# Performance work log

Measured on AMD Instinct MI355X. Metric: run time of the kernel, lower is better.

The kernel has to match this reference:

```python
import jax, jax.numpy as jnp
import numpy as np

EMBED_DIM = 4096
LOW_RANK = 512
BATCH = 8192
K_SEL = 128


def setup_inputs() -> dict:
    key = jax.random.key(0)
    k1, k2, k3, k4 = jax.random.split(key, 4)
    base = jax.random.normal(k1, (BATCH, EMBED_DIM), dtype=jnp.float32)
    source = jax.random.normal(k2, (BATCH, EMBED_DIM), dtype=jnp.float32)
    # fast path: only subspaces[0] is used (all examples share the same index set)
    row = jax.random.randint(k3, (1, K_SEL), 0, LOW_RANK)
    subspaces = jnp.broadcast_to(row, (BATCH, K_SEL)).astype(jnp.int64)
    # orthogonal (column-orthonormal) rotation weight, as produced by
    # torch.nn.utils.parametrizations.orthogonal on [embed_dim, low_rank]
    W, _ = jnp.linalg.qr(jax.random.normal(k4, (EMBED_DIM, LOW_RANK), dtype=jnp.float32))
    return {"base": base, "source": source, "subspaces": subspaces, "W": W}


def reference(base, source, subspaces, W):
    # rotated_base / rotated_source: [B, r]
    # diff in rotated space, gather selected subspace columns, project back.
    sel = subspaces[0]                      # [k] shared index set (fast path)
    diff = (source - base) @ W              # [B, r]
    diff_sel = diff[:, sel]                 # [B, k]
    W_sel = W[:, sel]                       # [d, k]
    out = base + diff_sel @ W_sel.T         # [B, d]
    return out.astype(base.dtype)
```

## Files before the change

### kernel.cpp

```cpp
#include <hip/hip_runtime.h>
#include <hip/hip_bf16.h>

typedef __attribute__((ext_vector_type(4))) float  f32x4;
typedef __attribute__((ext_vector_type(8))) short  short8;
typedef __attribute__((ext_vector_type(4))) short  short4v;

#define EMBED 4096
#define LR    512
#define KSEL  128
#define BATCH 8192
#define NSLICE 8
#define KSLICE 512

__device__ __forceinline__ short f2bf(float x) {
  union { float f; unsigned u; } c; c.f = x;
  unsigned r = c.u + 0x7FFFu + ((c.u >> 16) & 1u);
  return (short)(r >> 16);
}
__device__ __forceinline__ float bf2f(short s) {
  union { unsigned u; float f; } c; c.u = ((unsigned)(unsigned short)s) << 16;
  return c.f;
}
__device__ __forceinline__ void storept(float* p, float v) { *p = v; }
__device__ __forceinline__ void storept(short* p, float v) { *p = f2bf(v); }
__device__ __forceinline__ void loadpart(const float* p, f32x4& a, f32x4& b) {
  a += *(const f32x4*)p; b += *(const f32x4*)(p + 4);
}
__device__ __forceinline__ void loadpart(const short* p, f32x4& a, f32x4& b) {
  short8 v = *(const short8*)p;
  #pragma unroll
  for (int j = 0; j < 4; ++j) { a[j] += bf2f(v[j]); b[j] += bf2f(v[4 + j]); }
}

__global__ __launch_bounds__(256) void pack_w_kernel(
    const float* __restrict__ W, const int* __restrict__ sel,
    short* __restrict__ Wp, short* __restrict__ Wtp) {
  int idx = blockIdx.x * 256 + threadIdx.x;
  int e = idx >> 7;
  int c = idx & 127;
  int r = sel[c];
  short v = f2bf(W[e * LR + r]);
  Wp [(((e >> 3) << 7) + c) * 8 + (e & 7)] = v;
  Wtp[(((c >> 3) << 12) + e) * 8 + (c & 7)] = v;
}

template<typename PT>
__global__ __launch_bounds__(512, 4) void gemm1a_kernel(
    const float* __restrict__ base, const float* __restrict__ src,
    const short* __restrict__ Wp, PT* __restrict__ Tpart) {
  __shared__ __align__(16) short D[2 * 2048];
  const int t  = threadIdx.x;
  const int w  = t >> 6, l = t & 63;
  const int lr = l & 15, lg = l >> 4;
  const int rg = blockIdx.x & 63, slice = blockIdx.x >> 6;
  const int row0 = rg * 128;
  const int k0 = slice * KSLICE;

  short8 bfr[16];
  #pragma unroll
  for (int kg = 0; kg < 16; ++kg)
    bfr[kg] = *(const short8*)(Wp + (((((k0 >> 3) + kg * 4 + lg)) << 7) + w * 16 + lr) * 8);

  const int srow  = t >> 5;
  const int sbyte = srow * 256 + ((((t & 31) >> 1) ^ (srow & 7)) << 4) + (t & 1) * 8;
  const float* bp = base + (size_t)(row0 + srow) * EMBED + k0 + (t & 31) * 4;
  const float* sp = src  + (size_t)(row0 + srow) * EMBED + k0 + (t & 31) * 4;

  const int rsw = (lr & 7) << 4;
  const char* tb = (const char*)D + lr * 256;

  f32x4 vbA = *(const f32x4*)bp,          vsA = *(const f32x4*)sp;
  f32x4 vbB = *(const f32x4*)(bp + 128),  vsB = *(const f32x4*)(sp + 128);

  f32x4 acc = {0.f, 0.f, 0.f, 0.f};
  PT* tout = Tpart + (size_t)slice * BATCH * KSEL + (size_t)(row0 + lg * 4) * KSEL + w * 16 + lr;

  #define KSTEP(BUF, VB, VS, KG0, PF_OK, PF_OFF)                              \
    do {                                                                      \
      short4v d;                                                              \
      _Pragma("unroll")                                                       \
      for (int j = 0; j < 4; ++j) d[j] = f2bf(VS[j] - VB[j]);                 \
      *(short4v*)((char*)D + (BUF) * 4096 + sbyte) = d;                       \
      if (PF_OK) {                                                            \
        VB = *(const f32x4*)(bt + (PF_OFF));                                  \
        VS = *(const f32x4*)(st + (PF_OFF));                                  \
      }                                                                       \
      __syncthreads();                                                        \
      _Pragma("unroll")                                                       \
      for (int kg = 0; kg < 4; ++kg) {                                        \
        short8 a = *(const short8*)(tb + (BUF) * 4096 +                       \
                                    ((kg * 64 + lg * 16) ^ rsw));             \
        acc = __builtin_amdgcn_mfma_f32_16x16x32_bf16(a, bfr[(KG0) + kg],     \
                                                      acc, 0, 0, 0);          \
      }                                                                       \
    } while (0)

  for (int tile = 0; tile < 8; ++tile) {
    const float* bt = bp + (size_t)tile * 16 * EMBED;
    const float* st = sp + (size_t)tile * 16 * EMBED;
    const bool pf = (tile < 7);
    KSTEP(0, vbA, vsA, 0,  true, 256);
    KSTEP(1, vbB, vsB, 4,  true, 384);
    KSTEP(0, vbA, vsA, 8,  pf,   16 * EMBED);
    KSTEP(1, vbB, vsB, 12, pf,   16 * EMBED + 128);
    PT* o = tout + (size_t)tile * 16 * KSEL;
    #pragma unroll
    for (int r = 0; r < 4; ++r) storept(o + (size_t)r * KSEL, acc[r]);
    acc = (f32x4){0.f, 0.f, 0.f, 0.f};
  }
  #undef KSTEP
}

template<typename PT>
__global__ __launch_bounds__(512) void reduce_kernel(
    const PT* __restrict__ Tpart, short* __restrict__ Tp) {
  const int tid = blockIdx.x * 512 + threadIdx.x;
  const int kkg = tid & 15, row = tid >> 4;
  f32x4 s0 = {0.f, 0.f, 0.f, 0.f}, s1 = {0.f, 0.f, 0.f, 0.f};
  #pragma unroll
  for (int s = 0; s < NSLICE; ++s)
    loadpart(Tpart + ((size_t)s * BATCH + row) * KSEL + kkg * 8, s0, s1);
  short8 o;
  #pragma unroll
  for (int j = 0; j < 4; ++j) { o[j] = f2bf(s0[j]); o[4 + j] = f2bf(s1[j]); }
  *(short8*)(Tp + ((size_t)kkg * BATCH + row) * 8) = o;
}

__global__ __launch_bounds__(256) void gemm2_kernel(
    const float* __restrict__ base, const short* __restrict__ Tp,
    const short* __restrict__ Wtp, float* __restrict__ out) {
  const int t  = threadIdx.x;
  const int w  = t >> 6, l = t & 63;
  const int lr = l & 15, lg = l >> 4;
  const int mt = blockIdx.x >> 4, nt = blockIdx.x & 15;
  const int row0 = mt * 64;
  const int col0 = nt * 256 + w * 64;

  short8 afr[4][4];
  #pragma unroll
  for (int m = 0; m < 4; ++m)
    #pragma unroll
    for (int ks = 0; ks < 4; ++ks)
      afr[m][ks] = *(const short8*)(Tp + (size_t)(((ks * 4 + lg) << 13) + row0 + m * 16 + lr) * 8);

  f32x4 acc[4][4];
  #pragma unroll
  for (int m = 0; m < 4; ++m)
    #pragma unroll
    for (int nf = 0; nf < 4; ++nf) acc[m][nf] = (f32x4){0.f, 0.f, 0.f, 0.f};

  #pragma unroll
  for (int nf = 0; nf < 4; ++nf) {
    short8 bfr[4];
    #pragma unroll
    for (int ks = 0; ks < 4; ++ks)
      bfr[ks] = *(const short8*)(Wtp + (size_t)(((ks * 4 + lg) << 12) + col0 + nf * 16 + lr) * 8);
    #pragma unroll
    for (int m = 0; m < 4; ++m)
      #pragma unroll
      for (int ks = 0; ks < 4; ++ks)
        acc[m][nf] = __builtin_amdgcn_mfma_f32_16x16x32_bf16(afr[m][ks], bfr[ks], acc[m][nf], 0, 0, 0);
  }

  #pragma unroll
  for (int m = 0; m < 4; ++m)
    #pragma unroll
    for (int r = 0; r < 4; ++r) {
      const size_t row = row0 + m * 16 + lg * 4 + r;
      #pragma unroll
      for (int nf = 0; nf < 4; ++nf) {
        const size_t o = row * EMBED + col0 + nf * 16 + lr;
        out[o] = base[o] + acc[m][nf][r];
      }
    }
}

extern "C" void kernel_launch(void* const* d_in, const int* in_sizes, int n_in,
                              void* d_out, int out_size, void* d_ws, size_t ws_size,
                              hipStream_t stream) {
  const float* base = (const float*)d_in[0];
  const float* src  = (const float*)d_in[1];
  const int*   sub  = (const int*)d_in[2];
  const float* W    = (const float*)d_in[3];
  float* out = (float*)d_out;

  short* Wp  = (short*)d_ws;
  short* Wtp = Wp  + EMBED * KSEL;
  short* Tp  = Wtp + EMBED * KSEL;
  char*  rest = (char*)(Tp + BATCH * KSEL);

  pack_w_kernel<<<EMBED * KSEL / 256, 256, 0, stream>>>(W, sub, Wp, Wtp);

  const size_t need_f32 = (size_t)4 * 1024 * 1024 +
                          (size_t)NSLICE * BATCH * KSEL * sizeof(float);
  if (ws_size >= need_f32) {
    float* Tpart = (float*)rest;
    gemm1a_kernel<float><<<512, 512, 0, stream>>>(base, src, Wp, Tpart);
    reduce_kernel<float><<<BATCH * 16 / 512, 512, 0, stream>>>(Tpart, Tp);
  } else {
    short* Tpart = (short*)rest;
    gemm1a_kernel<short><<<512, 512, 0, stream>>>(base, src, Wp, Tpart);
    reduce_kernel<short><<<BATCH * 16 / 512, 512, 0, stream>>>(Tpart, Tp);
  }

  gemm2_kernel<<<(BATCH / 64) * 16, 256, 0, stream>>>(base, Tp, Wtp, out);
}
```

Measured before the change: 126.0 us.

## Load activation diff directly into MFMA A-fragments, dropping LDS staging in gemm1

```diff
diff --git a/kernel.cpp b/kernel.cpp
--- a/kernel.cpp
+++ b/kernel.cpp
@@ -3,7 +3,6 @@
 
 typedef __attribute__((ext_vector_type(4))) float  f32x4;
 typedef __attribute__((ext_vector_type(8))) short  short8;
-typedef __attribute__((ext_vector_type(4))) short  short4v;
 
 #define EMBED 4096
 #define LR    512
@@ -48,67 +47,45 @@
 __global__ __launch_bounds__(512, 4) void gemm1a_kernel(
     const float* __restrict__ base, const float* __restrict__ src,
     const short* __restrict__ Wp, PT* __restrict__ Tpart) {
-  __shared__ __align__(16) short D[2 * 2048];
   const int t  = threadIdx.x;
   const int w  = t >> 6, l = t & 63;
   const int lr = l & 15, lg = l >> 4;
   const int rg = blockIdx.x & 63, slice = blockIdx.x >> 6;
-  const int row0 = rg * 128;
+  const int row0 = rg * 128 + w * 16;
   const int k0 = slice * KSLICE;
 
-  short8 bfr[16];
+  const float* bp = base + (size_t)(row0 + lr) * EMBED + k0 + lg * 8;
+  const float* sp = src  + (size_t)(row0 + lr) * EMBED + k0 + lg * 8;
+  const short8* wq = (const short8*)Wp + ((k0 >> 3) + lg) * 128 + lr;
+
+  f32x4 acc[8];
   #pragma unroll
-  for (int kg = 0; kg < 16; ++kg)
-    bfr[kg] = *(const short8*)(Wp + (((((k0 >> 3) + kg * 4 + lg)) << 7) + w * 16 + lr) * 8);
+  for (int c = 0; c < 8; ++c) acc[c] = (f32x4){0.f, 0.f, 0.f, 0.f};
 
-  const int srow  = t >> 5;
-  const int sbyte = srow * 256 + ((((t & 31) >> 1) ^ (srow & 7)) << 4) + (t & 1) * 8;
-  const float* bp = base + (size_t)(row0 + srow) * EMBED + k0 + (t & 31) * 4;
-  const float* sp = src  + (size_t)(row0 + srow) * EMBED + k0 + (t & 31) * 4;
+  #pragma unroll
+  for (int ks = 0; ks < 16; ++ks) {
+    f32x4 b0 = *(const f32x4*)(bp + ks * 32);
+    f32x4 b1 = *(const f32x4*)(bp + ks * 32 + 4);
+    f32x4 s0 = *(const f32x4*)(sp + ks * 32);
+    f32x4 s1 = *(const f32x4*)(sp + ks * 32 + 4);
+    union { short8 v; __hip_bfloat162 h[4]; } ua;
+    ua.h[0] = __float22bfloat162_rn(make_float2(s0[0] - b0[0], s0[1] - b0[1]));
+    ua.h[1] = __float22bfloat162_rn(make_float2(s0[2] - b0[2], s0[3] - b0[3]));
+    ua.h[2] = __float22bfloat162_rn(make_float2(s1[0] - b1[0], s1[1] - b1[1]));
+    ua.h[3] = __float22bfloat162_rn(make_float2(s1[2] - b1[2], s1[3] - b1[3]));
+    #pragma unroll
+    for (int c = 0; c < 8; ++c) {
+      short8 bf = wq[ks * 512 + c * 16];
+      acc[c] = __builtin_amdgcn_mfma_f32_16x16x32_bf16(ua.v, bf, acc[c], 0, 0, 0);
+    }
+  }
 
-  const int rsw = (lr & 7) << 4;
-  const char* tb = (const char*)D + lr * 256;
-
-  f32x4 vbA = *(const f32x4*)bp,          vsA = *(const f32x4*)sp;
-  f32x4 vbB = *(const f32x4*)(bp + 128),  vsB = *(const f32x4*)(sp + 128);
-
-  f32x4 acc = {0.f, 0.f, 0.f, 0.f};
-  PT* tout = Tpart + (size_t)slice * BATCH * KSEL + (size_t)(row0 + lg * 4) * KSEL + w * 16 + lr;
-
-  #define KSTEP(BUF, VB, VS, KG0, PF_OK, PF_OFF)                              \
-    do {                                                                      \
-      short4v d;                                                              \
-      _Pragma("unroll")                                                       \
-      for (int j = 0; j < 4; ++j) d[j] = f2bf(VS[j] - VB[j]);                 \
-      *(short4v*)((char*)D + (BUF) * 4096 + sbyte) = d;                       \
-      if (PF_OK) {                                                            \
-        VB = *(const f32x4*)(bt + (PF_OFF));                                  \
-        VS = *(const f32x4*)(st + (PF_OFF));                                  \
-      }                                                                       \
-      __syncthreads();                                                        \
-      _Pragma("unroll")                                                       \
-      for (int kg = 0; kg < 4; ++kg) {                                        \
-        short8 a = *(const short8*)(tb + (BUF) * 4096 +                       \
-                                    ((kg * 64 + lg * 16) ^ rsw));             \
-        acc = __builtin_amdgcn_mfma_f32_16x16x32_bf16(a, bfr[(KG0) + kg],     \
-                                                      acc, 0, 0, 0);          \
-      }                                                                       \
-    } while (0)
-
-  for (int tile = 0; tile < 8; ++tile) {
-    const float* bt = bp + (size_t)tile * 16 * EMBED;
-    const float* st = sp + (size_t)tile * 16 * EMBED;
-    const bool pf = (tile < 7);
-    KSTEP(0, vbA, vsA, 0,  true, 256);
-    KSTEP(1, vbB, vsB, 4,  true, 384);
-    KSTEP(0, vbA, vsA, 8,  pf,   16 * EMBED);
-    KSTEP(1, vbB, vsB, 12, pf,   16 * EMBED + 128);
-    PT* o = tout + (size_t)tile * 16 * KSEL;
+  PT* o = Tpart + ((size_t)slice * BATCH + row0 + lg * 4) * KSEL + lr;
+  #pragma unroll
+  for (int c = 0; c < 8; ++c)
     #pragma unroll
-    for (int r = 0; r < 4; ++r) storept(o + (size_t)r * KSEL, acc[r]);
-    acc = (f32x4){0.f, 0.f, 0.f, 0.f};
-  }
-  #undef KSTEP
+    for (int r = 0; r < 4; ++r)
+      storept(o + (size_t)r * KSEL + c * 16, acc[c][r]);
 }
 
 template<typename PT>
```

Measured after the change: 142.7 us. +13.2%, slower.
